# Performance work log

Hardware: AMD Instinct MI355X
Metric: run time of the kernel (lower is better)

## Reference

```python
import jax, jax.numpy as jnp
import numpy as np

BOS_IDX = 1


def setup_inputs() -> dict:
    key = jax.random.key(0)
    ks = jax.random.split(key, 12)
    B, T, S, H, L, V = 16, 128, 64, 512, 2, 32000
    s = 0.05
    return {
        "encoder_outputs": jax.random.normal(ks[0], (B, S, H), jnp.float32),
        "encoder_h": jax.random.normal(ks[1], (L, B, H), jnp.float32) * s,
        "encoder_c": jax.random.normal(ks[2], (L, B, H), jnp.float32) * s,
        "target_tensor": jax.random.randint(ks[3], (B, T), 0, V),
        "embedding": jax.random.normal(ks[4], (V, H), jnp.float32) * s,
        "W_ih": jax.random.normal(ks[5], (L, 4 * H, H), jnp.float32) * s,
        "W_hh": jax.random.normal(ks[6], (L, 4 * H, H), jnp.float32) * s,
        "b_ih": jax.random.normal(ks[7], (L, 4 * H), jnp.float32) * s,
        "b_hh": jax.random.normal(ks[8], (L, 4 * H), jnp.float32) * s,
        "W_out": jax.random.normal(ks[9], (V, H), jnp.float32) * s,
        "b_out": jax.random.normal(ks[10], (V,), jnp.float32) * s,
    }


def reference(encoder_outputs, encoder_h, encoder_c, target_tensor,
              embedding, W_ih, W_hh, b_ih, b_hh, W_out, b_out):
    B, T = target_tensor.shape
    L = W_ih.shape[0]
    # Teacher-forced inputs: BOS then target[:, :-1]
    tokens = jnp.concatenate(
        [jnp.full((B, 1), BOS_IDX, dtype=target_tensor.dtype),
         target_tensor[:, :-1]], axis=1)  # [B, T]
    x = jax.nn.relu(embedding[tokens])  # [B, T, H]
    # The original loop resets (h, c) to encoder_states at EVERY step, so all
    # T single-step LSTM cells are independent -> vectorize over T.
    h_last, c_last = [], []
    for l in range(L):
        h0 = encoder_h[l]  # [B, H]
        c0 = encoder_c[l][:, None, :]  # [B, 1, H]
        gates = (jnp.einsum('bth,gh->btg', x, W_ih[l]) + b_ih[l]
                 + (jnp.einsum('bh,gh->bg', h0, W_hh[l]) + b_hh[l])[:, None, :])
        i, f, g, o = jnp.split(gates, 4, axis=-1)  # torch gate order i,f,g,o
        c = jax.nn.sigmoid(f) * c0 + jax.nn.sigmoid(i) * jnp.tanh(g)
        h = jax.nn.sigmoid(o) * jnp.tanh(c)  # [B, T, H]
        h_last.append(h[:, -1, :])
        c_last.append(c[:, -1, :])
        x = h  # input to next layer (dropout=0 / eval)
    logits = jnp.einsum('bth,vh->btv', x, W_out) + b_out  # [B, T, V]
    return logits, (jnp.stack(h_last), jnp.stack(c_last))
```

## Files before the change

kernel.cpp:

```cpp
#include <hip/hip_runtime.h>
#include <hip/hip_bf16.h>

typedef __bf16 bf16_t;
typedef __bf16 bf16x8 __attribute__((ext_vector_type(8)));
typedef __bf16 bf16x4 __attribute__((ext_vector_type(4)));
typedef float f32x4 __attribute__((ext_vector_type(4)));

#define B_ 16
#define T_ 128
#define H_ 512
#define L_ 2
#define V_ 32000
#define G_ 2048
#define M_ 2048

#define BM 128
#define BN 128
#define BK 32

__device__ __forceinline__ float sigf(float x) { return 1.f / (1.f + __expf(-x)); }
__device__ __forceinline__ float tanhf_(float x) { return 2.f / (1.f + __expf(-2.f * x)) - 1.f; }


__global__ __launch_bounds__(256) void prep(const float* __restrict__ emb,
                                            const int* __restrict__ target,
                                            const float* __restrict__ enc_h,
                                            const float* __restrict__ W_ih,
                                            const float* __restrict__ W_hh,
                                            const float* __restrict__ b_ih,
                                            const float* __restrict__ b_hh,
                                            const float* __restrict__ W_out,
                                            bf16_t* __restrict__ x,
                                            bf16_t* __restrict__ wih_b,
                                            bf16_t* __restrict__ wout_b,
                                            float* __restrict__ biasall) {
    const int blk = blockIdx.x;
    const int tid = threadIdx.x;
    if (blk < 256) {
        int idx = blk * 256 + tid;
        int b = idx & 15;
        int c = (idx >> 4) & (G_ - 1);
        int l = idx >> 15;
        int gate = (c >> 4) & 3;
        int h = ((c >> 6) << 4) | (c & 15);
        int r = gate * H_ + h;
        const float* hrow = enc_h + ((size_t)l * B_ + b) * H_;
        const float* wrow = W_hh + ((size_t)l * G_ + r) * H_;
        float acc = b_ih[l * G_ + r] + b_hh[l * G_ + r];
        #pragma unroll 4
        for (int k = 0; k < H_; k += 4) {
            float4 hv = *(const float4*)(hrow + k);
            float4 wv = *(const float4*)(wrow + k);
            acc += hv.x * wv.x + hv.y * wv.y + hv.z * wv.z + hv.w * wv.w;
        }
        biasall[((size_t)l * B_ + b) * G_ + c] = acc;
    } else if (blk < 2304) {
        int idx = (blk - 256) * 256 + tid;
        int k4 = idx & 127;
        int c  = (idx >> 7) & (G_ - 1);
        int l  = idx >> 18;
        int gate = (c >> 4) & 3;
        int h = ((c >> 6) << 4) | (c & 15);
        int r = gate * H_ + h;
        float4 v = *(const float4*)(W_ih + ((size_t)l * G_ + r) * H_ + k4 * 4);
        bf16x4 o;
        o[0] = (bf16_t)v.x; o[1] = (bf16_t)v.y; o[2] = (bf16_t)v.z; o[3] = (bf16_t)v.w;
        *(bf16x4*)(wih_b + ((size_t)l * G_ + c) * H_ + k4 * 4) = o;
    } else if (blk < 3328) {
        int idx = (blk - 2304) * 256 + tid;
        int m  = idx >> 7;
        int h4 = (idx & 127) << 2;
        int b = m >> 7, t = m & 127;
        int tok = (t == 0) ? 1 : target[b * T_ + t - 1];
        float4 v = *(const float4*)(emb + (size_t)tok * H_ + h4);
        bf16x4 o;
        o[0] = (bf16_t)fmaxf(v.x, 0.f);
        o[1] = (bf16_t)fmaxf(v.y, 0.f);
        o[2] = (bf16_t)fmaxf(v.z, 0.f);
        o[3] = (bf16_t)fmaxf(v.w, 0.f);
        *(bf16x4*)(x + (size_t)m * H_ + h4) = o;
    } else {
        int idx = (blk - 3328) * 256 + tid;
        float4 v = ((const float4*)W_out)[idx];
        bf16x4 o;
        o[0] = (bf16_t)v.x; o[1] = (bf16_t)v.y; o[2] = (bf16_t)v.z; o[3] = (bf16_t)v.w;
        ((bf16x4*)wout_b)[idx] = o;
    }
}

__global__ __launch_bounds__(256) void gemm_bt(const bf16_t* __restrict__ A,
                                               const bf16_t* __restrict__ B,
                                               float* __restrict__ C,
                                               const float* __restrict__ bias,
                                               int M, int N, int K, int mode,
                                               const float* __restrict__ enc_c,
                                               bf16_t* __restrict__ xout,
                                               float* __restrict__ out_h,
                                               float* __restrict__ out_c,
                                               int l) {
    __shared__ __align__(16) bf16_t As[BM * BK];
    __shared__ __align__(16) bf16_t Bs[BN * BK];

    const int tid  = threadIdx.x;
    const int lane = tid & 63;
    const int wave = tid >> 6;
    const int wm = wave >> 1, wn = wave & 1;
    const int quad = lane >> 4;
    const int r16  = lane & 15;

    const int nwg = gridDim.x;
    const int q = nwg >> 3;
    const int wg = (blockIdx.x & 7) * q + (blockIdx.x >> 3);
    const int bx = wg & 15;
    const int by = wg >> 4;
    const int tileM = bx * BM;
    const int tileN = by * BN;

    const int srow = lane >> 2;
    const int scol = (lane & 3) * 8;

    f32x4 acc[4][4];
    #pragma unroll
    for (int i = 0; i < 4; i++)
        #pragma unroll
        for (int j = 0; j < 4; j++) acc[i][j] = (f32x4){0.f, 0.f, 0.f, 0.f};

    const int nk = K / BK;
    for (int kt = 0; kt < nk; ++kt) {
        const int k0 = kt * BK;
        #pragma unroll
        for (int j = 0; j < 2; ++j) {
            const int r0 = j * 64 + wave * 16;
            const bf16_t* ga = A + (size_t)(tileM + r0 + srow) * K + k0 + scol;
            const bf16_t* gb = B + (size_t)(tileN + r0 + srow) * K + k0 + scol;
            __builtin_amdgcn_global_load_lds(
                (const __attribute__((address_space(1))) void*)ga,
                (__attribute__((address_space(3))) void*)(As + r0 * BK), 16, 0, 0);
            __builtin_amdgcn_global_load_lds(
                (const __attribute__((address_space(1))) void*)gb,
                (__attribute__((address_space(3))) void*)(Bs + r0 * BK), 16, 0, 0);
        }
        __syncthreads();

        bf16x8 af[4], bfr[4];
        #pragma unroll
        for (int mi = 0; mi < 4; mi++)
            af[mi] = *(const bf16x8*)(As + (wm * 64 + mi * 16 + r16) * BK + quad * 8);
        #pragma unroll
        for (int ni = 0; ni < 4; ni++)
            bfr[ni] = *(const bf16x8*)(Bs + (wn * 64 + ni * 16 + r16) * BK + quad * 8);
        #pragma unroll
        for (int mi = 0; mi < 4; mi++)
            #pragma unroll
            for (int ni = 0; ni < 4; ni++)
                acc[mi][ni] = __builtin_amdgcn_mfma_f32_16x16x32_bf16(
                    af[mi], bfr[ni], acc[mi][ni], 0, 0, 0);
        __syncthreads();
    }

    if (mode == 0) {
        #pragma unroll
        for (int mi = 0; mi < 4; mi++) {
            #pragma unroll
            for (int ni = 0; ni < 4; ni++) {
                const int col = tileN + wn * 64 + ni * 16 + r16;
                const float bv = bias[col];
                #pragma unroll
                for (int rr = 0; rr < 4; rr++) {
                    const int row = tileM + wm * 64 + mi * 16 + quad * 4 + rr;
                    __builtin_nontemporal_store(acc[mi][ni][rr] + bv,
                                                &C[(size_t)row * N + col]);
                }
            }
        }
    } else {
        const int b = bx;
        const float* brow = bias + (size_t)b * G_;
        float bv[4];
        #pragma unroll
        for (int g = 0; g < 4; g++)
            bv[g] = brow[tileN + wn * 64 + g * 16 + r16];
        const int h = (2 * by + wn) * 16 + r16;
        const float c0 = enc_c[((size_t)l * B_ + b) * H_ + h];
        #pragma unroll
        for (int mi = 0; mi < 4; mi++) {
            #pragma unroll
            for (int rr = 0; rr < 4; rr++) {
                const int t = wm * 64 + mi * 16 + quad * 4 + rr;
                const float gi = acc[mi][0][rr] + bv[0];
                const float gf = acc[mi][1][rr] + bv[1];
                const float gg = acc[mi][2][rr] + bv[2];
                const float go = acc[mi][3][rr] + bv[3];
                const float c = sigf(gf) * c0 + sigf(gi) * tanhf_(gg);
                const float hv = sigf(go) * tanhf_(c);
                xout[(size_t)(b * T_ + t) * H_ + h] = (bf16_t)hv;
                if (t == T_ - 1) {
                    out_h[((size_t)l * B_ + b) * H_ + h] = hv;
                    out_c[((size_t)l * B_ + b) * H_ + h] = c;
                }
            }
        }
    }
}

extern "C" void kernel_launch(void* const* d_in, const int* in_sizes, int n_in,
                              void* d_out, int out_size, void* d_ws, size_t ws_size,
                              hipStream_t stream) {
    const float* enc_h  = (const float*)d_in[1];
    const float* enc_c  = (const float*)d_in[2];
    const int*   target = (const int*)d_in[3];
    const float* emb    = (const float*)d_in[4];
    const float* W_ih   = (const float*)d_in[5];
    const float* W_hh   = (const float*)d_in[6];
    const float* b_ih   = (const float*)d_in[7];
    const float* b_hh   = (const float*)d_in[8];
    const float* W_out  = (const float*)d_in[9];
    const float* b_out  = (const float*)d_in[10];
    float* out = (float*)d_out;

    char* w = (char*)d_ws;
    bf16_t* x       = (bf16_t*)(w);
    bf16_t* wih_b   = (bf16_t*)(w + 2097152);
    bf16_t* wout_b  = (bf16_t*)(w + 6291456);
    bf16_t* x2      = (bf16_t*)(w + 39059456);
    float*  biasall = (float*)(w + 55836672);

    float* out_h = out + (size_t)M_ * V_;
    float* out_c = out_h + (size_t)L_ * B_ * H_;

    prep<<<19328, 256, 0, stream>>>(emb, target, enc_h, W_ih, W_hh, b_ih, b_hh,
                                    W_out, x, wih_b, wout_b, biasall);

    gemm_bt<<<(M_ / BM) * (G_ / BN), 256, 0, stream>>>(
        x, wih_b, (float*)x2, biasall, M_, G_, H_, 1,
        enc_c, x2, out_h, out_c, 0);
    gemm_bt<<<(M_ / BM) * (G_ / BN), 256, 0, stream>>>(
        x2, wih_b + (size_t)G_ * H_, (float*)x, biasall + (size_t)B_ * G_,
        M_, G_, H_, 1, enc_c, x, out_h, out_c, 1);

    gemm_bt<<<(M_ / BM) * (V_ / BN), 256, 0, stream>>>(
        x, wout_b, out, b_out, M_, V_, H_, 0,
        nullptr, nullptr, nullptr, nullptr, 0);
}
```

Measured before the change: 497.9 us.

## Double K tile, XOR-swizzle LDS, and use smaller M tiles for LSTM GEMMs

The K tile grows from 32 to 64, so the loop runs half as many iterations and issues half as many barriers. Shared-memory loads from global memory are now XOR-swizzled by row to avoid LDS bank conflicts. The kernel is templated on M tile size and mode: the two LSTM gate GEMMs use 64-row tiles, which doubles their block count for better occupancy of the CUs, while the output projection keeps 128-row tiles. The added LDS usage and index arithmetic may reduce occupancy slightly.

```diff
diff --git a/kernel.cpp b/kernel.cpp
--- a/kernel.cpp
+++ b/kernel.cpp
@@ -14,9 +14,8 @@
 #define G_ 2048
 #define M_ 2048
 
-#define BM 128
 #define BN 128
-#define BK 32
+#define BK 64
 
 __device__ __forceinline__ float sigf(float x) { return 1.f / (1.f + __expf(-x)); }
 __device__ __forceinline__ float tanhf_(float x) { return 2.f / (1.f + __expf(-2.f * x)) - 1.f; }
@@ -88,17 +87,21 @@
     }
 }
 
+template<int BMt, int MODE>
 __global__ __launch_bounds__(256) void gemm_bt(const bf16_t* __restrict__ A,
                                                const bf16_t* __restrict__ B,
                                                float* __restrict__ C,
                                                const float* __restrict__ bias,
-                                               int M, int N, int K, int mode,
+                                               int M, int N, int K,
                                                const float* __restrict__ enc_c,
                                                bf16_t* __restrict__ xout,
                                                float* __restrict__ out_h,
                                                float* __restrict__ out_c,
                                                int l) {
-    __shared__ __align__(16) bf16_t As[BM * BK];
+    constexpr int MIc = BMt / 32;
+    constexpr int NA  = BMt / 8;
+    constexpr int NB  = BN / 8;
+    __shared__ __align__(16) bf16_t As[BMt * BK];
     __shared__ __align__(16) bf16_t Bs[BN * BK];
 
     const int tid  = threadIdx.x;
@@ -109,19 +112,20 @@
     const int r16  = lane & 15;
 
     const int nwg = gridDim.x;
-    const int q = nwg >> 3;
+    const int q  = nwg >> 3;
     const int wg = (blockIdx.x & 7) * q + (blockIdx.x >> 3);
-    const int bx = wg & 15;
-    const int by = wg >> 4;
-    const int tileM = bx * BM;
+    const int nbx = M / BMt;
+    const int bx = wg % nbx;
+    const int by = wg / nbx;
+    const int tileM = bx * BMt;
     const int tileN = by * BN;
 
-    const int srow = lane >> 2;
-    const int scol = (lane & 3) * 8;
-
-    f32x4 acc[4][4];
+    const int srow = lane >> 3;
+    const int scol = (((lane & 7) ^ (lane >> 3)) << 3);
+
+    f32x4 acc[MIc][4];
     #pragma unroll
-    for (int i = 0; i < 4; i++)
+    for (int i = 0; i < MIc; i++)
         #pragma unroll
         for (int j = 0; j < 4; j++) acc[i][j] = (f32x4){0.f, 0.f, 0.f, 0.f};
 
@@ -129,52 +133,66 @@
     for (int kt = 0; kt < nk; ++kt) {
         const int k0 = kt * BK;
         #pragma unroll
-        for (int j = 0; j < 2; ++j) {
-            const int r0 = j * 64 + wave * 16;
-            const bf16_t* ga = A + (size_t)(tileM + r0 + srow) * K + k0 + scol;
-            const bf16_t* gb = B + (size_t)(tileN + r0 + srow) * K + k0 + scol;
+        for (int ii = 0; ii < (NA + NB) / 4; ++ii) {
+            const int i = ii * 4 + wave;
+            const bf16_t* src;
+            bf16_t* dst;
+            if (i < NA) {
+                const int r0 = i * 8;
+                src = A + (size_t)(tileM + r0 + srow) * K + k0 + scol;
+                dst = As + r0 * BK;
+            } else {
+                const int r0 = (i - NA) * 8;
+                src = B + (size_t)(tileN + r0 + srow) * K + k0 + scol;
+                dst = Bs + r0 * BK;
+            }
             __builtin_amdgcn_global_load_lds(
-                (const __attribute__((address_space(1))) void*)ga,
-                (__attribute__((address_space(3))) void*)(As + r0 * BK), 16, 0, 0);
-            __builtin_amdgcn_global_load_lds(
-                (const __attribute__((address_space(1))) void*)gb,
-                (__attribute__((address_space(3))) void*)(Bs + r0 * BK), 16, 0, 0);
+                (const __attribute__((address_space(1))) void*)src,
+                (__attribute__((address_space(3))) void*)dst, 16, 0, 0);
         }
         __syncthreads();
 
-        bf16x8 af[4], bfr[4];
-        #pragma unroll
-        for (int mi = 0; mi < 4; mi++)
-            af[mi] = *(const bf16x8*)(As + (wm * 64 + mi * 16 + r16) * BK + quad * 8);
-        #pragma unroll
-        for (int ni = 0; ni < 4; ni++)
-            bfr[ni] = *(const bf16x8*)(Bs + (wn * 64 + ni * 16 + r16) * BK + quad * 8);
-        #pragma unroll
-        for (int mi = 0; mi < 4; mi++)
-            #pragma unroll
-            for (int ni = 0; ni < 4; ni++)
-                acc[mi][ni] = __builtin_amdgcn_mfma_f32_16x16x32_bf16(
-                    af[mi], bfr[ni], acc[mi][ni], 0, 0, 0);
+        #pragma unroll
+        for (int ks = 0; ks < 2; ++ks) {
+            bf16x8 af[MIc], bfr[4];
+            const int ub = ks * 4 + quad;
+            #pragma unroll
+            for (int mi = 0; mi < MIc; mi++) {
+                const int row = wm * (BMt / 2) + mi * 16 + r16;
+                af[mi] = *(const bf16x8*)(As + row * BK + ((ub ^ (r16 & 7)) << 3));
+            }
+            #pragma unroll
+            for (int ni = 0; ni < 4; ni++) {
+                const int row = wn * 64 + ni * 16 + r16;
+                bfr[ni] = *(const bf16x8*)(Bs + row * BK + ((ub ^ (r16 & 7)) << 3));
+            }
+            #pragma unroll
+            for (int mi = 0; mi < MIc; mi++)
+                #pragma unroll
+                for (int ni = 0; ni < 4; ni++)
+                    acc[mi][ni] = __builtin_amdgcn_mfma_f32_16x16x32_bf16(
+                        af[mi], bfr[ni], acc[mi][ni], 0, 0, 0);
+        }
         __syncthreads();
     }
 
-    if (mode == 0) {
-        #pragma unroll
-        for (int mi = 0; mi < 4; mi++) {
+    if (MODE == 0) {
+        #pragma unroll
+        for (int mi = 0; mi < MIc; mi++) {
             #pragma unroll
             for (int ni = 0; ni < 4; ni++) {
                 const int col = tileN + wn * 64 + ni * 16 + r16;
                 const float bv = bias[col];
                 #pragma unroll
                 for (int rr = 0; rr < 4; rr++) {
-                    const int row = tileM + wm * 64 + mi * 16 + quad * 4 + rr;
+                    const int row = tileM + wm * (BMt / 2) + mi * 16 + quad * 4 + rr;
                     __builtin_nontemporal_store(acc[mi][ni][rr] + bv,
                                                 &C[(size_t)row * N + col]);
                 }
             }
         }
     } else {
-        const int b = bx;
+        const int b = tileM >> 7;
         const float* brow = bias + (size_t)b * G_;
         float bv[4];
         #pragma unroll
@@ -183,10 +201,10 @@
         const int h = (2 * by + wn) * 16 + r16;
         const float c0 = enc_c[((size_t)l * B_ + b) * H_ + h];
         #pragma unroll
-        for (int mi = 0; mi < 4; mi++) {
+        for (int mi = 0; mi < MIc; mi++) {
             #pragma unroll
             for (int rr = 0; rr < 4; rr++) {
-                const int t = wm * 64 + mi * 16 + quad * 4 + rr;
+                const int t = (tileM & 127) + wm * (BMt / 2) + mi * 16 + quad * 4 + rr;
                 const float gi = acc[mi][0][rr] + bv[0];
                 const float gf = acc[mi][1][rr] + bv[1];
                 const float gg = acc[mi][2][rr] + bv[2];
@@ -231,14 +249,14 @@
     prep<<<19328, 256, 0, stream>>>(emb, target, enc_h, W_ih, W_hh, b_ih, b_hh,
                                     W_out, x, wih_b, wout_b, biasall);
 
-    gemm_bt<<<(M_ / BM) * (G_ / BN), 256, 0, stream>>>(
-        x, wih_b, (float*)x2, biasall, M_, G_, H_, 1,
+    gemm_bt<64, 1><<<(M_ / 64) * (G_ / BN), 256, 0, stream>>>(
+        x, wih_b, nullptr, biasall, M_, G_, H_,
         enc_c, x2, out_h, out_c, 0);
-    gemm_bt<<<(M_ / BM) * (G_ / BN), 256, 0, stream>>>(
-        x2, wih_b + (size_t)G_ * H_, (float*)x, biasall + (size_t)B_ * G_,
-        M_, G_, H_, 1, enc_c, x, out_h, out_c, 1);
-
-    gemm_bt<<<(M_ / BM) * (V_ / BN), 256, 0, stream>>>(
-        x, wout_b, out, b_out, M_, V_, H_, 0,
+    gemm_bt<64, 1><<<(M_ / 64) * (G_ / BN), 256, 0, stream>>>(
+        x2, wih_b + (size_t)G_ * H_, nullptr, biasall + (size_t)B_ * G_,
+        M_, G_, H_, enc_c, x, out_h, out_c, 1);
+
+    gemm_bt<128, 0><<<(M_ / 128) * (V_ / BN), 256, 0, stream>>>(
+        x, wout_b, out, b_out, M_, V_, H_,
         nullptr, nullptr, nullptr, nullptr, 0);
 }
```

Measured after the change: 454.4 us. -8.7%, faster.
